# Kernel optimization log

Hardware: AMD Instinct MI355X
Metric: run time of the kernel (lower is better)

The kernel has to match this reference:

```python
import jax, jax.numpy as jnp
import numpy as np

B, D, K0, K1 = 262144, 128, 50, 1  # batch, embed dim, cluster-space k, noise-space k


def setup_inputs() -> dict:
    key = jax.random.key(0)
    k_z, k_v, k_c0, k_c1 = jax.random.split(key, 4)
    z = jax.random.normal(k_z, (B, D), dtype=jnp.float32)
    # beta_weights_init with P=[range(0,64), range(64,128)], high_value=0.9
    high = 0.9
    on = np.float32(np.log(1.0 / high - 1.0))
    off = np.float32(np.log(1.0 / (1.0 - high) - 1.0))
    bw = np.full((2, D), off, dtype=np.float32)
    bw[0, : D // 2] = on
    bw[1, D // 2 :] = on
    beta_weights = jnp.asarray(bw)
    # orthogonal rotation matrix V (ENRC assumption: V^T V = I)
    V, _ = jnp.linalg.qr(jax.random.normal(k_v, (D, D), dtype=jnp.float32))
    centers0 = jax.random.normal(k_c0, (K0, D), dtype=jnp.float32)
    centers1 = jax.random.normal(k_c1, (K1, D), dtype=jnp.float32)
    return {"z": z, "beta_weights": beta_weights, "V": V,
            "centers0": centers0, "centers1": centers1}


def _weighted_sqdist(z_rot, centers, beta):
    # sum_d beta_d * (z_d - c_d)^2  =  (z^2)·beta + (c^2)·beta - 2 (z*beta) @ c^T
    zz = (z_rot * z_rot) @ beta          # [B]
    cc = (centers * centers) @ beta      # [K]
    cross = (z_rot * beta) @ centers.T   # [B, K]
    return zz[:, None] + cc[None, :] - 2.0 * cross


def reference(z, beta_weights, V, centers0, centers1):
    # soft subspace dimension assignments (softmax over sub-clusterings)
    betas = jax.nn.softmax(beta_weights, axis=0)      # [2, D]
    z_rot = z @ V                                     # rotate embeddings, [B, D]
    d0 = _weighted_sqdist(z_rot, centers0, betas[0])  # [B, K0]
    d1 = _weighted_sqdist(z_rot, centers1, betas[1])  # [B, K1]
    return jnp.concatenate([d0, d1], axis=1)          # [B, K0+K1]
```

## Files before the change

### kernel.cpp

```cpp
#include <hip/hip_runtime.h>
#include <hip/hip_bf16.h>

#define D     128
#define K0    50
#define NCOL  51
#define NT    12
#define TB    256

typedef __attribute__((ext_vector_type(4))) float  f32x4;
typedef __attribute__((ext_vector_type(8))) short  short8x;
typedef f32x4 __attribute__((aligned(4))) f32x4u;
typedef __attribute__((ext_vector_type(2))) float f32x2;
typedef f32x2 __attribute__((aligned(4))) f32x2u;

__device__ inline short f2bf(float x) {
    __hip_bfloat16 h = __float2bfloat16(x);
    return __builtin_bit_cast(short, h);
}

__global__ __launch_bounds__(128) void setup_kernel(
    const float* __restrict__ bw,
    const float* __restrict__ V,
    const float* __restrict__ c0,
    const float* __restrict__ c1,
    short* __restrict__ Gws,
    float* __restrict__ ccws,
    float* __restrict__ betaws)
{
    const int blk = blockIdx.x;
    const int t   = threadIdx.x;
    __shared__ float beta0[D];
    __shared__ float Vt[D * 33];
    __shared__ float wct[D * 17];

    if (t < D) {
        float b0 = bw[t], b1 = bw[D + t];
        beta0[t] = 1.0f / (1.0f + expf(b1 - b0));
    }
    __syncthreads();

    if (blk == 48) {
        if (t < D) betaws[t] = beta0[t];
        if (t < NCOL) {
            const float* cr = (t < K0) ? (c0 + (size_t)t * D) : c1;
            float s = 0.f;
            for (int e = 0; e < D; ++e) {
                float b = (t == K0) ? (1.0f - beta0[e]) : beta0[e];
                float cv = cr[e];
                s += b * cv * cv;
            }
            ccws[t] = s;
        }
        return;
    }

    const int kstep = blk / NT;
    const int ntile = blk % NT;
    const int lane  = t >> 1;
    const int jbase = (t & 1) * 4;
    const int nl    = lane & 15;

    if (ntile < 8) {
        const int n = ntile * 16 + nl;
        short* dst = Gws + ((size_t)(blk * 64 + lane)) * 8 + jbase;
        for (int jj = 0; jj < 4; ++jj) {
            int d = kstep * 32 + (lane >> 4) * 8 + jbase + jj;
            dst[jj] = f2bf(V[(size_t)d * D + n]);
        }
        return;
    }

    for (int i = t; i < 32 * D; i += 128) {
        int d = i >> 7, e = i & 127;
        Vt[e * 33 + d] = V[(size_t)(kstep * 32 + d) * D + e];
    }
    for (int i = t; i < 16 * D; i += 128) {
        int kl = i >> 7, e = i & 127;
        int k = (ntile - 8) * 16 + kl;
        float w = 0.f;
        if (k < K0)       w = beta0[e] * c0[(size_t)k * D + e];
        else if (k == K0) w = (1.0f - beta0[e]) * c1[e];
        wct[e * 17 + kl] = w;
    }
    __syncthreads();

    short res[4];
    for (int jj = 0; jj < 4; ++jj) {
        int dl = (lane >> 4) * 8 + jbase + jj;
        float s = 0.f;
        #pragma unroll 8
        for (int e = 0; e < D; ++e)
            s += Vt[e * 33 + dl] * wct[e * 17 + nl];
        res[jj] = f2bf(-2.0f * s);
    }
    short* dst = Gws + ((size_t)(blk * 64 + lane)) * 8 + jbase;
    for (int jj = 0; jj < 4; ++jj) dst[jj] = res[jj];
}

__global__ __launch_bounds__(256, 3) void main_kernel(
    const float* __restrict__ z,
    const short* __restrict__ Gws,
    const float* __restrict__ ccws,
    const float* __restrict__ betaws,
    float* __restrict__ out)
{
    __shared__ __align__(16) short Gs[48 * 64 * 8];

    const int t    = threadIdx.x;
    const int wave = t >> 6;
    const int lane = t & 63;
    const int c    = lane & 15;
    const int q    = lane >> 4;
    const size_t rowbase = (size_t)blockIdx.x * TB;

    for (int i = t; i < 48 * 64 * 8 / 8; i += 256)
        ((int4*)Gs)[i] = ((const int4*)Gws)[i];

    float breg[8];
    #pragma unroll
    for (int nt = 0; nt < 8; ++nt) breg[nt] = betaws[nt * 16 + c];
    float ccreg[4][4];
    #pragma unroll
    for (int j = 0; j < 4; ++j)
        #pragma unroll
        for (int r = 0; r < 4; ++r) {
            int kk = j * 16 + q * 4 + r;
            ccreg[j][r] = (kk <= K0) ? ccws[kk] : 0.f;
        }
    __syncthreads();

    for (int rt = 0; rt < 4; ++rt) {
        const int rowloc = (wave * 4 + rt) * 16;
        const float* zrow = z + (rowbase + rowloc + c) * D;

        short8x zfrag[4];
        float nrm_p = 0.f;
        #pragma unroll
        for (int ks = 0; ks < 4; ++ks) {
            const float* p = zrow + ks * 32 + q * 8;
            f32x4 v0 = *(const f32x4*)p;
            f32x4 v1 = *(const f32x4*)(p + 4);
            nrm_p += v0.x*v0.x + v0.y*v0.y + v0.z*v0.z + v0.w*v0.w
                   + v1.x*v1.x + v1.y*v1.y + v1.z*v1.z + v1.w*v1.w;
            short8x a;
            a[0] = f2bf(v0.x); a[1] = f2bf(v0.y); a[2] = f2bf(v0.z); a[3] = f2bf(v0.w);
            a[4] = f2bf(v1.x); a[5] = f2bf(v1.y); a[6] = f2bf(v1.z); a[7] = f2bf(v1.w);
            zfrag[ks] = a;
        }

        f32x4 accr[8], accc[4];
        #pragma unroll
        for (int nt = 0; nt < 8; ++nt) accr[nt] = f32x4{0.f, 0.f, 0.f, 0.f};
        #pragma unroll
        for (int j = 0; j < 4; ++j)   accc[j]  = f32x4{0.f, 0.f, 0.f, 0.f};

        #pragma unroll
        for (int ks = 0; ks < 4; ++ks) {
            #pragma unroll
            for (int nt = 0; nt < 8; ++nt) {
                short8x bfrg = *(const short8x*)&Gs[((ks * NT + nt) * 64 + lane) * 8];
                accr[nt] = __builtin_amdgcn_mfma_f32_16x16x32_bf16(zfrag[ks], bfrg, accr[nt], 0, 0, 0);
            }
            #pragma unroll
            for (int j = 0; j < 4; ++j) {
                short8x afrg = *(const short8x*)&Gs[((ks * NT + 8 + j) * 64 + lane) * 8];
                accc[j] = __builtin_amdgcn_mfma_f32_16x16x32_bf16(afrg, zfrag[ks], accc[j], 0, 0, 0);
            }
        }

        float qp[4] = {0.f, 0.f, 0.f, 0.f};
        #pragma unroll
        for (int nt = 0; nt < 8; ++nt) {
            #pragma unroll
            for (int r = 0; r < 4; ++r) {
                float y = accr[nt][r];
                qp[r] += breg[nt] * y * y;
            }
        }
        #pragma unroll
        for (int s = 1; s < 16; s <<= 1) {
            #pragma unroll
            for (int r = 0; r < 4; ++r) qp[r] += __shfl_xor(qp[r], s, 64);
        }
        float nrm = nrm_p + __shfl_xor(nrm_p, 16, 64);
        nrm += __shfl_xor(nrm, 32, 64);

        float tq[4];
        const int srcl = (c >> 2) * 16;
        #pragma unroll
        for (int r = 0; r < 4; ++r) tq[r] = __shfl(qp[r], srcl, 64);
        float zz0 = (c & 2) ? ((c & 1) ? tq[3] : tq[2])
                            : ((c & 1) ? tq[1] : tq[0]);

        float* orow = out + (rowbase + rowloc + c) * NCOL;
        #pragma unroll
        for (int j = 0; j < 3; ++j) {
            f32x4 v;
            #pragma unroll
            for (int r = 0; r < 4; ++r) v[r] = zz0 + ccreg[j][r] + accc[j][r];
            *(f32x4u*)(orow + j * 16 + q * 4) = v;
        }
        if (q == 0) {
            f32x2 v2;
            v2.x = zz0 + ccreg[3][0] + accc[3][0];
            v2.y = zz0 + ccreg[3][1] + accc[3][1];
            *(f32x2u*)(orow + 48) = v2;
            orow[50] = (nrm - zz0) + ccreg[3][2] + accc[3][2];
        }
    }
}

extern "C" void kernel_launch(void* const* d_in, const int* in_sizes, int n_in,
                              void* d_out, int out_size, void* d_ws, size_t ws_size,
                              hipStream_t stream) {
    const float* z  = (const float*)d_in[0];
    const float* bw = (const float*)d_in[1];
    const float* V  = (const float*)d_in[2];
    const float* c0 = (const float*)d_in[3];
    const float* c1 = (const float*)d_in[4];
    float* out = (float*)d_out;

    short* Gws    = (short*)d_ws;
    float* ccws   = (float*)((char*)d_ws + 48 * 64 * 8 * 2);
    float* betaws = ccws + 64;

    const int B = in_sizes[0] / D;

    setup_kernel<<<49, 128, 0, stream>>>(bw, V, c0, c1, Gws, ccws, betaws);
    main_kernel<<<B / TB, 256, 0, stream>>>(z, Gws, ccws, betaws, out);
}
```

Before: 233.1 us.

## Shrink LDS tile set, read cluster tiles 10-11 from global, fold cc into acc

Only 10 of the 12 G tiles per k-step are staged in shared memory. The last two cluster-distance tiles are read directly from global (L2/L1) inside the MFMA loop. The cc offsets now initialise the accumulators instead of being held in 16 registers, and ccws is zero-padded to 64 entries. Together with raising launch bounds to 4 blocks per SM, this aims for higher occupancy to better hide z load latency, at the cost of extra global loads in the inner loop.

Result: slower. 388.1 us (+66.5%).

```diff
diff --git a/kernel.cpp b/kernel.cpp
--- a/kernel.cpp
+++ b/kernel.cpp
@@ -5,6 +5,7 @@
 #define K0    50
 #define NCOL  51
 #define NT    12
+#define NLT   10
 #define TB    256
 
 typedef __attribute__((ext_vector_type(4))) float  f32x4;
@@ -41,6 +42,7 @@
 
     if (blk == 48) {
         if (t < D) betaws[t] = beta0[t];
+        if (t >= NCOL && t < 64) ccws[t] = 0.f;
         if (t < NCOL) {
             const float* cr = (t < K0) ? (c0 + (size_t)t * D) : c1;
             float s = 0.f;
@@ -97,14 +99,14 @@
     for (int jj = 0; jj < 4; ++jj) dst[jj] = res[jj];
 }
 
-__global__ __launch_bounds__(256, 3) void main_kernel(
+__global__ __launch_bounds__(256, 4) void main_kernel(
     const float* __restrict__ z,
     const short* __restrict__ Gws,
     const float* __restrict__ ccws,
     const float* __restrict__ betaws,
     float* __restrict__ out)
 {
-    __shared__ __align__(16) short Gs[48 * 64 * 8];
+    __shared__ __align__(16) short Gs[4 * NLT * 64 * 8];
 
     const int t    = threadIdx.x;
     const int wave = t >> 6;
@@ -113,20 +115,15 @@
     const int q    = lane >> 4;
     const size_t rowbase = (size_t)blockIdx.x * TB;
 
-    for (int i = t; i < 48 * 64 * 8 / 8; i += 256)
-        ((int4*)Gs)[i] = ((const int4*)Gws)[i];
+    for (int i = t; i < 4 * NLT * 64; i += 256) {
+        int m = i >> 6, r = i & 63;
+        int g = (m / NLT) * NT + (m % NLT);
+        ((int4*)Gs)[i] = ((const int4*)Gws)[g * 64 + r];
+    }
 
     float breg[8];
     #pragma unroll
     for (int nt = 0; nt < 8; ++nt) breg[nt] = betaws[nt * 16 + c];
-    float ccreg[4][4];
-    #pragma unroll
-    for (int j = 0; j < 4; ++j)
-        #pragma unroll
-        for (int r = 0; r < 4; ++r) {
-            int kk = j * 16 + q * 4 + r;
-            ccreg[j][r] = (kk <= K0) ? ccws[kk] : 0.f;
-        }
     __syncthreads();
 
     for (int rt = 0; rt < 4; ++rt) {
@@ -152,18 +149,24 @@
         #pragma unroll
         for (int nt = 0; nt < 8; ++nt) accr[nt] = f32x4{0.f, 0.f, 0.f, 0.f};
         #pragma unroll
-        for (int j = 0; j < 4; ++j)   accc[j]  = f32x4{0.f, 0.f, 0.f, 0.f};
+        for (int j = 0; j < 4; ++j)
+            accc[j] = *(const f32x4*)(ccws + j * 16 + q * 4);
 
         #pragma unroll
         for (int ks = 0; ks < 4; ++ks) {
             #pragma unroll
             for (int nt = 0; nt < 8; ++nt) {
-                short8x bfrg = *(const short8x*)&Gs[((ks * NT + nt) * 64 + lane) * 8];
+                short8x bfrg = *(const short8x*)&Gs[((ks * NLT + nt) * 64 + lane) * 8];
                 accr[nt] = __builtin_amdgcn_mfma_f32_16x16x32_bf16(zfrag[ks], bfrg, accr[nt], 0, 0, 0);
             }
             #pragma unroll
-            for (int j = 0; j < 4; ++j) {
-                short8x afrg = *(const short8x*)&Gs[((ks * NT + 8 + j) * 64 + lane) * 8];
+            for (int j = 0; j < 2; ++j) {
+                short8x afrg = *(const short8x*)&Gs[((ks * NLT + 8 + j) * 64 + lane) * 8];
+                accc[j] = __builtin_amdgcn_mfma_f32_16x16x32_bf16(afrg, zfrag[ks], accc[j], 0, 0, 0);
+            }
+            #pragma unroll
+            for (int j = 2; j < 4; ++j) {
+                short8x afrg = *(const short8x*)&Gws[((size_t)((ks * NT + 8 + j) * 64 + lane)) * 8];
                 accc[j] = __builtin_amdgcn_mfma_f32_16x16x32_bf16(afrg, zfrag[ks], accc[j], 0, 0, 0);
             }
         }
@@ -197,15 +200,15 @@
         for (int j = 0; j < 3; ++j) {
             f32x4 v;
             #pragma unroll
-            for (int r = 0; r < 4; ++r) v[r] = zz0 + ccreg[j][r] + accc[j][r];
+            for (int r = 0; r < 4; ++r) v[r] = zz0 + accc[j][r];
             *(f32x4u*)(orow + j * 16 + q * 4) = v;
         }
         if (q == 0) {
             f32x2 v2;
-            v2.x = zz0 + ccreg[3][0] + accc[3][0];
-            v2.y = zz0 + ccreg[3][1] + accc[3][1];
+            v2.x = zz0 + accc[3][0];
+            v2.y = zz0 + accc[3][1];
             *(f32x2u*)(orow + 48) = v2;
-            orow[50] = (nrm - zz0) + ccreg[3][2] + accc[3][2];
+            orow[50] = (nrm - zz0) + accc[3][2];
         }
     }
 }
```
